# Kernel optimization log

Hardware: AMD Instinct MI355X
Metric: run time of the kernel (lower is better)

## Reference

```python
import jax, jax.numpy as jnp
import numpy as np

N, M, K, C, FF, H, OUT = 20000, 80000, 48, 64, 256, 4, 64


def _lin(x, w, b):
    return x @ w.T + b


def _bn(x, g, b, eps=1e-5):
    mu = x.mean(0)
    var = x.var(0)
    return (x - mu) * jax.lax.rsqrt(var + eps) * g + b


def setup_inputs() -> dict:
    key = jax.random.key(0)
    ks = jax.random.split(key, 24)
    voxel_features = jax.random.normal(ks[0], (M, C), jnp.float32)
    voxel_coords = jax.random.normal(ks[1], (M, 3), jnp.float32)
    query_coords = jax.random.normal(ks[2], (N, 3), jnp.float32)
    idx = jax.random.randint(ks[3], (N, K), 0, M)
    drop = jax.random.uniform(ks[4], (N, K)) < 0.1
    drop = drop.at[:, 0].set(False)  # keep >=1 valid key per query
    key_indices = jnp.where(drop, -1, idx)
    s = 0.05
    p = lambda i, shp: jax.random.normal(ks[i], shp, jnp.float32) * s
    return {
        "voxel_features": voxel_features,
        "voxel_coords": voxel_coords,
        "query_coords": query_coords,
        "key_indices": key_indices,
        "q_w": p(5, (C, 3)), "q_b": p(6, (C,)),
        "kpos_w": p(7, (C, 3)), "kpos_b": p(8, (C,)),
        "in_w": p(9, (3 * C, C)), "in_b": p(10, (3 * C,)),
        "out_w": p(11, (C, C)), "out_b": p(12, (C,)),
        "lin1_w": p(13, (FF, C)), "lin1_b": p(14, (FF,)),
        "lin2_w": p(15, (C, FF)), "lin2_b": p(16, (C,)),
        "norm_g": jnp.ones((C,), jnp.float32), "norm_b": jnp.zeros((C,), jnp.float32),
        "outl_w": p(17, (OUT, C)), "outl_b": p(18, (OUT,)),
        "obn_g": jnp.ones((OUT,), jnp.float32), "obn_b": jnp.zeros((OUT,), jnp.float32),
    }


def reference(voxel_features, voxel_coords, query_coords, key_indices,
              q_w, q_b, kpos_w, kpos_b, in_w, in_b, out_w, out_b,
              lin1_w, lin1_b, lin2_w, lin2_b, norm_g, norm_b,
              outl_w, outl_b, obn_g, obn_b):
    hd = C // H
    mask = key_indices < 0                      # (N,K) padded keys
    safe = jnp.where(mask, 0, key_indices)
    key_feats = voxel_features[safe]            # (N,K,C) hash-gather
    key_coords = voxel_coords[safe]             # (N,K,3)
    # query positional projection
    q_feat = jax.nn.relu(_lin(query_coords, q_w, q_b))          # (N,C)
    # relative coords + key positional conv1d(kernel=1) == linear on coord dim
    rel = key_coords - query_coords[:, None, :]                  # (N,K,3)
    key_feats = key_feats + jax.nn.relu(_lin(rel, kpos_w, kpos_b))
    # multihead attention, query length 1 per voxel
    Wq, Wk, Wv = jnp.split(in_w, 3, axis=0)
    bq, bk, bv = jnp.split(in_b, 3)
    q = (_lin(q_feat, Wq, bq) / jnp.sqrt(jnp.float32(hd))).reshape(N, H, hd)
    k = _lin(key_feats, Wk, bk).reshape(N, K, H, hd)
    v = _lin(key_feats, Wv, bv).reshape(N, K, H, hd)
    scores = jnp.einsum('nhd,nkhd->nhk', q, k)
    scores = jnp.where(mask[:, None, :], -jnp.inf, scores)
    attn = jax.nn.softmax(scores, axis=-1)
    ctx = jnp.einsum('nhk,nkhd->nhd', attn, v).reshape(N, C)
    att = _lin(ctx, out_w, out_b)                                # (N,C)
    # FFN + residual
    x = att + _lin(jax.nn.relu(_lin(att, lin1_w, lin1_b)), lin2_w, lin2_b)
    x = _bn(x, norm_g, norm_b)
    # output layer: Linear -> BN -> ReLU
    x = jax.nn.relu(_bn(_lin(x, outl_w, outl_b), obn_g, obn_b))
    return x
```

## Files before the change

kernel.cpp:

```cpp
#include <hip/hip_runtime.h>
#include <math.h>

#define N_Q 20000
#define KK 48
#define CC 64
#define FFD 256

#define TW_WOB   0
#define TW_WVT   4096
#define TW_L1B   8192
#define TW_L2B   16384
#define TW_OLB   24576
#define TW_QB    26624
#define TW_KB    28672
#define ST_OFF   32768
#define M_OFF    33024
#define VF_OFF   2593024

typedef short bf16x8 __attribute__((ext_vector_type(8)));
typedef float f32x4  __attribute__((ext_vector_type(4)));

__device__ __forceinline__ unsigned pk2(float a, float b) {
    unsigned r;
    asm("v_cvt_pk_bf16_f32 %0, %1, %2" : "=v"(r) : "v"(a), "v"(b));
    return r;
}
__device__ __forceinline__ unsigned f2bf(float a) {
    unsigned r;
    asm("v_cvt_pk_bf16_f32 %0, %1, 0" : "=v"(r) : "v"(a));
    return r & 0xffffu;
}
__device__ __forceinline__ float bflo(unsigned u) { return __uint_as_float(u << 16); }
__device__ __forceinline__ float bfhi(unsigned u) { return __uint_as_float(u & 0xffff0000u); }
__device__ __forceinline__ bf16x8 ldfrag(const unsigned short* p) {
    return *(const bf16x8*)p;
}

__global__ void prep_all(const float* __restrict__ in_w,
                         const float* __restrict__ out_w,
                         const float* __restrict__ lin1_w,
                         const float* __restrict__ lin2_w,
                         const float* __restrict__ outl_w,
                         const float* __restrict__ vfeat,
                         float* __restrict__ tw,
                         unsigned short* __restrict__ vfeat_bf,
                         float* __restrict__ stats)
{
    int t = blockIdx.x * 256 + threadIdx.x;
    unsigned* twu = (unsigned*)tw;
    if (t < 1280000) {
        float4 v = ((const float4*)vfeat)[t];
        uint2 p; p.x = pk2(v.x, v.y); p.y = pk2(v.z, v.w);
        ((uint2*)vfeat_bf)[t] = p;
    }
    if (t < 256) stats[t] = 0.0f;
    if (t < 4096) {
        if (t < 2048) {
            int p = t;
            int j2 = p & 3, lane = (p >> 2) & 63, nb = (p >> 8) & 3, ks = p >> 10;
            int nn = nb*16 + (lane & 15), k = ks*32 + (lane >> 4)*8 + 2*j2;
            twu[TW_WOB + p] = pk2(out_w[nn*64 + k], out_w[nn*64 + k + 1]);
        }
    } else if (t < 8192) {
        if (t < 6144) {
            int p = t - 4096;
            int j2 = p & 3, lane = (p >> 2) & 63, nb = (p >> 8) & 3, ks = p >> 10;
            int nn = nb*16 + (lane & 15), k = ks*32 + (lane >> 4)*8 + 2*j2;
            twu[TW_WVT + p] = pk2(in_w[(128 + nn)*64 + k], in_w[(128 + nn)*64 + k + 1]);
        }
    } else if (t < 16384) {
        int p = t - 8192;
        int j2 = p & 3, lane = (p >> 2) & 63, nb = (p >> 8) & 15, ks = p >> 12;
        int n = nb*16 + (lane & 15), k = ks*32 + (lane >> 4)*8 + 2*j2;
        twu[TW_L1B + p] = pk2(lin1_w[n*64 + k], lin1_w[n*64 + k + 1]);
    } else if (t < 24576) {
        int p = t - 16384;
        int j2 = p & 3, lane = (p >> 2) & 63, nb = (p >> 8) & 3, ks = p >> 10;
        int n = nb*16 + (lane & 15), k = ks*32 + (lane >> 4)*8 + 2*j2;
        twu[TW_L2B + p] = pk2(lin2_w[n*256 + k], lin2_w[n*256 + k + 1]);
    } else if (t < 26624) {
        int p = t - 24576;
        int j2 = p & 3, lane = (p >> 2) & 63, nb = (p >> 8) & 3, ks = p >> 10;
        int n = nb*16 + (lane & 15), k = ks*32 + (lane >> 4)*8 + 2*j2;
        twu[TW_OLB + p] = pk2(outl_w[n*64 + k], outl_w[n*64 + k + 1]);
    } else if (t < 28672) {
        int p = t - 26624;
        int j2 = p & 3, lane = (p >> 2) & 63, nb = (p >> 8) & 3, ks = p >> 10;
        int n = nb*16 + (lane & 15), k = ks*32 + (lane >> 4)*8 + 2*j2;
        twu[TW_QB + p] = pk2(in_w[n*64 + k], in_w[n*64 + k + 1]);
    } else if (t < 32768) {
        int p = t - 28672;
        int j2 = p & 3, lane = (p >> 2) & 63, nb = (p >> 8) & 3, h = p >> 10;
        int j = nb*16 + (lane & 15), k = (lane >> 4)*8 + 2*j2;
        unsigned u = 0;
        if (k < 16)
            u = pk2(in_w[(64 + h*16 + k)*64 + j], in_w[(64 + h*16 + k + 1)*64 + j]);
        twu[TW_KB + p] = u;
    }
}

__global__ __launch_bounds__(256) void m_kernel(
    const float* __restrict__ qcoord, const float* __restrict__ q_w,
    const float* __restrict__ q_b, const float* __restrict__ in_b,
    const float* __restrict__ tw, unsigned short* __restrict__ M_all)
{
    __shared__ __align__(16) unsigned short sQF[80*72];
    __shared__ __align__(16) unsigned short sQ[80*72];
    int t = threadIdx.x, base = blockIdx.x * 80;
    int colq = (t*4) & 63;
    float qwv[12];
    #pragma unroll
    for (int j = 0; j < 12; ++j) qwv[j] = q_w[colq*3 + j];
    float4 qb4 = *(const float4*)&q_b[colq];
    #pragma unroll
    for (int i = 0; i < 5; ++i) {
        int e = i*1024 + t*4, r = e >> 6, n = base + r;
        float c0 = qcoord[n*3], c1 = qcoord[n*3+1], c2 = qcoord[n*3+2];
        float f0 = fmaxf(fmaf(qwv[2],  c2, fmaf(qwv[1],  c1, fmaf(qwv[0], c0, qb4.x))), 0.f);
        float f1 = fmaxf(fmaf(qwv[5],  c2, fmaf(qwv[4],  c1, fmaf(qwv[3], c0, qb4.y))), 0.f);
        float f2 = fmaxf(fmaf(qwv[8],  c2, fmaf(qwv[7],  c1, fmaf(qwv[6], c0, qb4.z))), 0.f);
        float f3 = fmaxf(fmaf(qwv[11], c2, fmaf(qwv[10], c1, fmaf(qwv[9], c0, qb4.w))), 0.f);
        uint2 p; p.x = pk2(f0, f1); p.y = pk2(f2, f3);
        *(uint2*)&sQF[r*72 + colq] = p;
    }
    int w = t >> 6, lane = t & 63, l16 = lane & 15, quad = lane >> 4;
    const unsigned* QB = (const unsigned*)(tw + TW_QB);
    const unsigned* KB = (const unsigned*)(tw + TW_KB);
    bf16x8 qbf[2], kbf[4];
    #pragma unroll
    for (int ks = 0; ks < 2; ++ks)
        qbf[ks] = ldfrag((const unsigned short*)&QB[((ks*4 + w)*64 + lane)*4]);
    #pragma unroll
    for (int nb = 0; nb < 4; ++nb)
        kbf[nb] = ldfrag((const unsigned short*)&KB[((w*4 + nb)*64 + lane)*4]);
    __syncthreads();

    int cq = w*16 + l16;
    float bq = in_b[cq];
    #pragma unroll
    for (int mb = 0; mb < 5; ++mb) {
        bf16x8 a0 = ldfrag(&sQF[(mb*16 + l16)*72 + quad*8]);
        bf16x8 a1 = ldfrag(&sQF[(mb*16 + l16)*72 + 32 + quad*8]);
        f32x4 acc = {0.f, 0.f, 0.f, 0.f};
        acc = __builtin_amdgcn_mfma_f32_16x16x32_bf16(a0, qbf[0], acc, 0, 0, 0);
        acc = __builtin_amdgcn_mfma_f32_16x16x32_bf16(a1, qbf[1], acc, 0, 0, 0);
        #pragma unroll
        for (int reg = 0; reg < 4; ++reg) {
            int row = mb*16 + quad*4 + reg;
            sQ[row*72 + cq] = (unsigned short)f2bf((acc[reg] + bq) * 0.25f);
        }
    }
    #pragma unroll
    for (int mb = 0; mb < 5; ++mb) {
        bf16x8 a = {0,0,0,0,0,0,0,0};
        if (quad < 2) a = ldfrag(&sQ[(mb*16 + l16)*72 + w*16 + quad*8]);
        f32x4 acc[4];
        #pragma unroll
        for (int nb = 0; nb < 4; ++nb) {
            f32x4 z = {0.f, 0.f, 0.f, 0.f};
            acc[nb] = __builtin_amdgcn_mfma_f32_16x16x32_bf16(a, kbf[nb], z, 0, 0, 0);
        }
        #pragma unroll
        for (int nb = 0; nb < 4; ++nb)
            #pragma unroll
            for (int reg = 0; reg < 4; ++reg) {
                int r = base + mb*16 + quad*4 + reg, j = nb*16 + l16;
                M_all[(size_t)r*256 + w*64 + j] = (unsigned short)f2bf(acc[nb][reg]);
            }
    }
}

__global__ __launch_bounds__(128, 4) void attn_kernel(
    const unsigned short* __restrict__ vfeat_bf, const float* __restrict__ vcoord,
    const float* __restrict__ qcoord, const int* __restrict__ kidx,
    const float* __restrict__ kpos_w, const float* __restrict__ kpos_b,
    const float* __restrict__ in_b,
    const float* __restrict__ tw, const unsigned short* __restrict__ M_all,
    float* __restrict__ ctx_out)
{
    __shared__ __align__(16) unsigned short skf2[2][KK*72];
    int wv = threadIdx.x >> 6, c = threadIdx.x & 63;
    int n = blockIdx.x * 2 + wv;
    unsigned short* skf = skf2[wv];
    int l16 = c & 15, quad = c >> 4;

    const unsigned short* Mrow = M_all + (size_t)n*256 + (l16 & 3)*64 + quad*8;
    bf16x8 mf0 = ldfrag(Mrow);
    bf16x8 mf1 = ldfrag(Mrow + 32);
    const unsigned* VBu = (const unsigned*)(tw + TW_WVT);
    bf16x8 wvf[2][4];
    #pragma unroll
    for (int ks = 0; ks < 2; ++ks)
        #pragma unroll
        for (int nb = 0; nb < 4; ++nb)
            wvf[ks][nb] = ldfrag((const unsigned short*)&VBu[((ks*4 + nb)*64 + c)*4]);

    float qc0 = qcoord[n*3+0], qc1 = qcoord[n*3+1], qc2 = qcoord[n*3+2];

    int kread = c < 48 ? c : 47;
    int idxv = kidx[(size_t)n*KK + kread];
    int sfe = idxv < 0 ? 0 : idxv;
    float rl0 = vcoord[sfe*3+0] - qc0;
    float rl1 = vcoord[sfe*3+1] - qc1;
    float rl2 = vcoord[sfe*3+2] - qc2;

    float4 wA  = *(const float4*)(kpos_w + 12*l16 + 0);
    float4 wB  = *(const float4*)(kpos_w + 12*l16 + 4);
    float4 wC  = *(const float4*)(kpos_w + 12*l16 + 8);
    float4 kb4 = *(const float4*)(kpos_b + 4*l16);

    uint2 fv[12];
    #pragma unroll
    for (int i = 0; i < 12; ++i) {
        int row = 4*i + quad;
        int si = __shfl(idxv, row);
        si = si < 0 ? 0 : si;
        fv[i] = *(const uint2*)(vfeat_bf + (size_t)si*64 + 4*l16);
    }
    #pragma unroll
    for (int i = 0; i < 12; ++i) {
        int row = 4*i + quad;
        float rr0 = __shfl(rl0, row), rr1 = __shfl(rl1, row), rr2 = __shfl(rl2, row);
        float g0 = bflo(fv[i].x), g1 = bfhi(fv[i].x);
        float g2 = bflo(fv[i].y), g3 = bfhi(fv[i].y);
        g0 += fmaxf(fmaf(wA.x, rr0, fmaf(wA.y, rr1, fmaf(wA.z, rr2, kb4.x))), 0.0f);
        g1 += fmaxf(fmaf(wA.w, rr0, fmaf(wB.x, rr1, fmaf(wB.y, rr2, kb4.y))), 0.0f);
        g2 += fmaxf(fmaf(wB.z, rr0, fmaf(wB.w, rr1, fmaf(wC.x, rr2, kb4.z))), 0.0f);
        g3 += fmaxf(fmaf(wC.y, rr0, fmaf(wC.z, rr1, fmaf(wC.w, rr2, kb4.w))), 0.0f);
        uint2 p; p.x = pk2(g0, g1); p.y = pk2(g2, g3);
        *(uint2*)&skf[row*72 + 4*l16] = p;
    }

    unsigned long long vm = __ballot(c < 48 && idxv >= 0);
    bf16x8 a0s[3], a1s[3];
    float S[3][4];
    #pragma unroll
    for (int mb = 0; mb < 3; ++mb) {
        a0s[mb] = ldfrag(&skf[(mb*16 + l16)*72 + quad*8]);
        a1s[mb] = ldfrag(&skf[(mb*16 + l16)*72 + 32 + quad*8]);
        f32x4 acc = {0.f, 0.f, 0.f, 0.f};
        acc = __builtin_amdgcn_mfma_f32_16x16x32_bf16(a0s[mb], mf0, acc, 0, 0, 0);
        acc = __builtin_amdgcn_mfma_f32_16x16x32_bf16(a1s[mb], mf1, acc, 0, 0, 0);
        #pragma unroll
        for (int r = 0; r < 4; ++r) {
            int kk = mb*16 + quad*4 + r;
            S[mb][r] = ((vm >> kk) & 1ull) ? acc[r] : -1e30f;
        }
    }

    float mx = S[0][0];
    #pragma unroll
    for (int mb = 0; mb < 3; ++mb)
        #pragma unroll
        for (int r = 0; r < 4; ++r) mx = fmaxf(mx, S[mb][r]);
    mx = fmaxf(mx, __shfl_xor(mx, 16));
    mx = fmaxf(mx, __shfl_xor(mx, 32));
    float p[3][4], es = 0.f;
    #pragma unroll
    for (int mb = 0; mb < 3; ++mb)
        #pragma unroll
        for (int r = 0; r < 4; ++r) { p[mb][r] = __expf(S[mb][r] - mx); es += p[mb][r]; }
    es += __shfl_xor(es, 16);
    es += __shfl_xor(es, 32);
    float rinv = 1.0f / es;
    #pragma unroll
    for (int mb = 0; mb < 3; ++mb)
        #pragma unroll
        for (int r = 0; r < 4; ++r) p[mb][r] *= rinv;

    float cacc0 = 0.f, cacc1 = 0.f, cacc2 = 0.f, cacc3 = 0.f;
    #pragma unroll
    for (int mb = 0; mb < 3; ++mb) {
        f32x4 av[4];
        #pragma unroll
        for (int nb = 0; nb < 4; ++nb) {
            f32x4 z = {0.f, 0.f, 0.f, 0.f};
            z = __builtin_amdgcn_mfma_f32_16x16x32_bf16(a0s[mb], wvf[0][nb], z, 0, 0, 0);
            av[nb] = __builtin_amdgcn_mfma_f32_16x16x32_bf16(a1s[mb], wvf[1][nb], z, 0, 0, 0);
        }
        #pragma unroll
        for (int r = 0; r < 4; ++r) {
            float pv = p[mb][r];
            float p0 = __shfl(pv, quad*16 + 0);
            float p1 = __shfl(pv, quad*16 + 1);
            float p2 = __shfl(pv, quad*16 + 2);
            float p3 = __shfl(pv, quad*16 + 3);
            cacc0 = fmaf(p0, av[0][r], cacc0);
            cacc1 = fmaf(p1, av[1][r], cacc1);
            cacc2 = fmaf(p2, av[2][r], cacc2);
            cacc3 = fmaf(p3, av[3][r], cacc3);
        }
    }
    cacc0 += __shfl_xor(cacc0, 16); cacc0 += __shfl_xor(cacc0, 32);
    cacc1 += __shfl_xor(cacc1, 16); cacc1 += __shfl_xor(cacc1, 32);
    cacc2 += __shfl_xor(cacc2, 16); cacc2 += __shfl_xor(cacc2, 32);
    cacc3 += __shfl_xor(cacc3, 16); cacc3 += __shfl_xor(cacc3, 32);
    float cv = quad == 0 ? cacc0 : quad == 1 ? cacc1 : quad == 2 ? cacc2 : cacc3;
    cv += in_b[128 + c];
    ctx_out[(size_t)n*64 + c] = cv;
}

__global__ __launch_bounds__(256) void ffn_kernel(
    const float* __restrict__ tw, const float* __restrict__ out_b,
    const float* __restrict__ lin1_b, const float* __restrict__ lin2_b,
    float* __restrict__ ctx_y,
    float* __restrict__ sum1, float* __restrict__ sumsq1)
{
    __shared__ __align__(16) unsigned short sA[80*72];
    __shared__ __align__(16) unsigned short sH[80*264];
    unsigned short* sC = sH;
    int t = threadIdx.x, base = blockIdx.x * 80;
    #pragma unroll
    for (int i = 0; i < 5; ++i) {
        int e = i*1024 + t*4, r = e >> 6, col = e & 63;
        float4 v = *(const float4*)&ctx_y[(size_t)(base + r)*64 + col];
        uint2 p; p.x = pk2(v.x, v.y); p.y = pk2(v.z, v.w);
        *(uint2*)&sC[r*72 + col] = p;
    }
    int w = t >> 6, lane = t & 63, l16 = lane & 15, quad = lane >> 4;
    const unsigned* WOB = (const unsigned*)(tw + TW_WOB);
    const unsigned* L1B = (const unsigned*)(tw + TW_L1B);
    const unsigned* L2B = (const unsigned*)(tw + TW_L2B);
    bf16x8 wob[2], b1f[2][4], b2f[8];
    #pragma unroll
    for (int ks = 0; ks < 2; ++ks)
        wob[ks] = ldfrag((const unsigned short*)&WOB[((ks*4 + w)*64 + lane)*4]);
    #pragma unroll
    for (int ks = 0; ks < 2; ++ks)
        #pragma unroll
        for (int nb = 0; nb < 4; ++nb)
            b1f[ks][nb] = ldfrag((const unsigned short*)&L1B[((ks*16 + w*4 + nb)*64 + lane)*4]);
    #pragma unroll
    for (int ks = 0; ks < 8; ++ks)
        b2f[ks] = ldfrag((const unsigned short*)&L2B[((ks*4 + w)*64 + lane)*4]);
    __syncthreads();

    int c = w*16 + l16;
    float ob = out_b[c];
    f32x4 attacc[5];
    #pragma unroll
    for (int mb = 0; mb < 5; ++mb) {
        bf16x8 a0 = ldfrag(&sC[(mb*16 + l16)*72 + quad*8]);
        bf16x8 a1 = ldfrag(&sC[(mb*16 + l16)*72 + 32 + quad*8]);
        f32x4 acc = {0.f, 0.f, 0.f, 0.f};
        acc = __builtin_amdgcn_mfma_f32_16x16x32_bf16(a0, wob[0], acc, 0, 0, 0);
        acc = __builtin_amdgcn_mfma_f32_16x16x32_bf16(a1, wob[1], acc, 0, 0, 0);
        #pragma unroll
        for (int reg = 0; reg < 4; ++reg) {
            float av = acc[reg] + ob;
            attacc[mb][reg] = av;
            int row = mb*16 + quad*4 + reg;
            sA[row*72 + c] = (unsigned short)f2bf(av);
        }
    }
    __syncthreads();

    #pragma unroll
    for (int mb = 0; mb < 5; ++mb) {
        bf16x8 a0 = ldfrag(&sA[(mb*16 + l16)*72 + quad*8]);
        bf16x8 a1 = ldfrag(&sA[(mb*16 + l16)*72 + 32 + quad*8]);
        #pragma unroll
        for (int nb = 0; nb < 4; ++nb) {
            f32x4 acc = {0.f, 0.f, 0.f, 0.f};
            acc = __builtin_amdgcn_mfma_f32_16x16x32_bf16(a0, b1f[0][nb], acc, 0, 0, 0);
            acc = __builtin_amdgcn_mfma_f32_16x16x32_bf16(a1, b1f[1][nb], acc, 0, 0, 0);
            int f = w*64 + nb*16 + l16;
            float bias = lin1_b[f];
            #pragma unroll
            for (int reg = 0; reg < 4; ++reg) {
                int row = mb*16 + quad*4 + reg;
                sH[row*264 + f] = (unsigned short)f2bf(fmaxf(acc[reg] + bias, 0.0f));
            }
        }
    }
    __syncthreads();

    float lb2 = lin2_b[c];
    float s = 0.f, ss = 0.f;
    #pragma unroll
    for (int mb = 0; mb < 5; ++mb) {
        f32x4 acc = {0.f, 0.f, 0.f, 0.f};
        #pragma unroll
        for (int ks = 0; ks < 8; ++ks) {
            bf16x8 a = ldfrag(&sH[(mb*16 + l16)*264 + ks*32 + quad*8]);
            acc = __builtin_amdgcn_mfma_f32_16x16x32_bf16(a, b2f[ks], acc, 0, 0, 0);
        }
        #pragma unroll
        for (int reg = 0; reg < 4; ++reg) {
            int r = base + mb*16 + quad*4 + reg;
            float y = attacc[mb][reg] + lb2 + acc[reg];
            ctx_y[(size_t)r*64 + c] = y;
            s += y; ss = fmaf(y, y, ss);
        }
    }
    s  += __shfl_xor(s, 16);  s  += __shfl_xor(s, 32);
    ss += __shfl_xor(ss, 16); ss += __shfl_xor(ss, 32);
    if (lane < 16) {
        atomicAdd(&sum1[c], s);
        atomicAdd(&sumsq1[c], ss);
    }
}

__global__ __launch_bounds__(256) void linout_kernel(
    const float* __restrict__ tw, const float* __restrict__ outl_b,
    const float* __restrict__ norm_g, const float* __restrict__ norm_b,
    const float* __restrict__ sum1, const float* __restrict__ sumsq1,
    const float* __restrict__ y, float* __restrict__ z_out,
    float* __restrict__ sum2, float* __restrict__ sumsq2)
{
    __shared__ __align__(16) unsigned short sX[80*72];
    int t = threadIdx.x, base = blockIdx.x * 80;
    int colq = (t*4) & 63;
    const float invN = 1.0f / 20000.0f;
    float4 sm = *(const float4*)&sum1[colq];
    float4 sq = *(const float4*)&sumsq1[colq];
    float4 g  = *(const float4*)&norm_g[colq];
    float4 bb = *(const float4*)&norm_b[colq];
    float mu0 = sm.x*invN, mu1 = sm.y*invN, mu2 = sm.z*invN, mu3 = sm.w*invN;
    float a0 = g.x / sqrtf(fmaf(-mu0, mu0, sq.x*invN) + 1e-5f);
    float a1 = g.y / sqrtf(fmaf(-mu1, mu1, sq.y*invN) + 1e-5f);
    float a2 = g.z / sqrtf(fmaf(-mu2, mu2, sq.z*invN) + 1e-5f);
    float a3 = g.w / sqrtf(fmaf(-mu3, mu3, sq.w*invN) + 1e-5f);
    float b0 = fmaf(-mu0, a0, bb.x), b1 = fmaf(-mu1, a1, bb.y);
    float b2 = fmaf(-mu2, a2, bb.z), b3 = fmaf(-mu3, a3, bb.w);
    #pragma unroll
    for (int i = 0; i < 5; ++i) {
        int e = i*1024 + t*4, r = e >> 6;
        float4 v = *(const float4*)&y[(size_t)(base + r)*64 + colq];
        uint2 p;
        p.x = pk2(fmaf(v.x, a0, b0), fmaf(v.y, a1, b1));
        p.y = pk2(fmaf(v.z, a2, b2), fmaf(v.w, a3, b3));
        *(uint2*)&sX[r*72 + colq] = p;
    }
    int w = t >> 6, lane = t & 63, l16 = lane & 15, quad = lane >> 4;
    const unsigned* OLB = (const unsigned*)(tw + TW_OLB);
    bf16x8 obf[2];
    #pragma unroll
    for (int ks = 0; ks < 2; ++ks)
        obf[ks] = ldfrag((const unsigned short*)&OLB[((ks*4 + w)*64 + lane)*4]);
    __syncthreads();

    int co = w*16 + l16;
    float ob = outl_b[co];
    float s = 0.f, ss = 0.f;
    #pragma unroll
    for (int mb = 0; mb < 5; ++mb) {
        bf16x8 x0 = ldfrag(&sX[(mb*16 + l16)*72 + quad*8]);
        bf16x8 x1 = ldfrag(&sX[(mb*16 + l16)*72 + 32 + quad*8]);
        f32x4 acc = {0.f, 0.f, 0.f, 0.f};
        acc = __builtin_amdgcn_mfma_f32_16x16x32_bf16(x0, obf[0], acc, 0, 0, 0);
        acc = __builtin_amdgcn_mfma_f32_16x16x32_bf16(x1, obf[1], acc, 0, 0, 0);
        #pragma unroll
        for (int reg = 0; reg < 4; ++reg) {
            int r = base + mb*16 + quad*4 + reg;
            float zv = acc[reg] + ob;
            z_out[(size_t)r*64 + co] = zv;
            s += zv; ss = fmaf(zv, zv, ss);
        }
    }
    s  += __shfl_xor(s, 16);  s  += __shfl_xor(s, 32);
    ss += __shfl_xor(ss, 16); ss += __shfl_xor(ss, 32);
    if (lane < 16) {
        atomicAdd(&sum2[co], s);
        atomicAdd(&sumsq2[co], ss);
    }
}

__global__ void final_kernel(float* __restrict__ z,
    const float* __restrict__ sum2, const float* __restrict__ sumsq2,
    const float* __restrict__ obn_g, const float* __restrict__ obn_b)
{
    int i = blockIdx.x*blockDim.x + threadIdx.x;
    if (i >= N_Q*64/4) return;
    int o4 = (i*4) & 63;
    float4 sm = *(const float4*)&sum2[o4];
    float4 sq = *(const float4*)&sumsq2[o4];
    float4 g  = *(const float4*)&obn_g[o4];
    float4 b  = *(const float4*)&obn_b[o4];
    const float invN = 1.0f / 20000.0f;
    float mux = sm.x*invN, muy = sm.y*invN, muz = sm.z*invN, muw = sm.w*invN;
    float ax = g.x / sqrtf(fmaf(-mux, mux, sq.x*invN) + 1e-5f);
    float ay = g.y / sqrtf(fmaf(-muy, muy, sq.y*invN) + 1e-5f);
    float az = g.z / sqrtf(fmaf(-muz, muz, sq.z*invN) + 1e-5f);
    float aw = g.w / sqrtf(fmaf(-muw, muw, sq.w*invN) + 1e-5f);
    float4 v = ((float4*)z)[i];
    v.x = fmaxf(fmaf(v.x - mux, ax, b.x), 0.0f);
    v.y = fmaxf(fmaf(v.y - muy, ay, b.y), 0.0f);
    v.z = fmaxf(fmaf(v.z - muz, az, b.z), 0.0f);
    v.w = fmaxf(fmaf(v.w - muw, aw, b.w), 0.0f);
    ((float4*)z)[i] = v;
}

extern "C" void kernel_launch(void* const* d_in, const int* in_sizes, int n_in,
                              void* d_out, int out_size, void* d_ws, size_t ws_size,
                              hipStream_t stream)
{
    const float* vfeat  = (const float*)d_in[0];
    const float* vcoord = (const float*)d_in[1];
    const float* qcoord = (const float*)d_in[2];
    const int*   kidx   = (const int*)d_in[3];
    const float* q_w    = (const float*)d_in[4];
    const float* q_b    = (const float*)d_in[5];
    const float* kpos_w = (const float*)d_in[6];
    const float* kpos_b = (const float*)d_in[7];
    const float* in_w   = (const float*)d_in[8];
    const float* in_b   = (const float*)d_in[9];
    const float* out_w  = (const float*)d_in[10];
    const float* out_b  = (const float*)d_in[11];
    const float* lin1_w = (const float*)d_in[12];
    const float* lin1_b = (const float*)d_in[13];
    const float* lin2_w = (const float*)d_in[14];
    const float* lin2_b = (const float*)d_in[15];
    const float* norm_g = (const float*)d_in[16];
    const float* norm_b = (const float*)d_in[17];
    const float* outl_w = (const float*)d_in[18];
    const float* outl_b = (const float*)d_in[19];
    const float* obn_g  = (const float*)d_in[20];
    const float* obn_b  = (const float*)d_in[21];

    float* ws = (float*)d_ws;
    float* tw = ws;
    float* stats = ws + ST_OFF;
    float* sum1 = stats, *sumsq1 = stats + 64, *sum2 = stats + 128, *sumsq2 = stats + 192;
    unsigned short* M_all = (unsigned short*)(ws + M_OFF);
    unsigned short* vfeat_bf = (unsigned short*)(ws + VF_OFF);
    float* xd = (float*)d_out;

    prep_all<<<5120, 256, 0, stream>>>(in_w, out_w, lin1_w, lin2_w, outl_w,
                                       vfeat, tw, vfeat_bf, stats);
    m_kernel<<<250, 256, 0, stream>>>(qcoord, q_w, q_b, in_b, tw, M_all);
    attn_kernel<<<N_Q/2, 128, 0, stream>>>(vfeat_bf, vcoord, qcoord, kidx, kpos_w,
                                           kpos_b, in_b, tw, M_all, xd);
    ffn_kernel<<<250, 256, 0, stream>>>(tw, out_b, lin1_b, lin2_b, xd, sum1, sumsq1);
    linout_kernel<<<250, 256, 0, stream>>>(tw, outl_b, norm_g, norm_b, sum1, sumsq1,
                                           xd, xd, sum2, sumsq2);
    final_kernel<<<1250, 256, 0, stream>>>(xd, sum2, sumsq2, obn_g, obn_b);
}
```

Before: 174.9 us.

## Fuse FFN, output linear and BatchNorms into one cooperative grid-synced kernel

Merges the FFN, output-linear and final BN/ReLU kernels into a single cooperative kernel. It keeps per-block activations in registers and LDS across two grid-wide syncs, which serve as barriers for the batch-norm statistics. This removes two kernel launches and two full round trips of the intermediate activations through global memory. The attention kernel's key-feature gather also changes, from 8-byte to 16-byte loads per lane with 8 channels each. The cost is that all 250 blocks must be co-resident, and the grid syncs add barrier latency.

```diff
diff --git a/kernel.cpp b/kernel.cpp
--- a/kernel.cpp
+++ b/kernel.cpp
@@ -1,5 +1,8 @@
 #include <hip/hip_runtime.h>
+#include <hip/hip_cooperative_groups.h>
 #include <math.h>
+
+namespace cg = cooperative_groups;
 
 #define N_Q 20000
 #define KK 48
@@ -34,6 +37,9 @@
 __device__ __forceinline__ float bfhi(unsigned u) { return __uint_as_float(u & 0xffff0000u); }
 __device__ __forceinline__ bf16x8 ldfrag(const unsigned short* p) {
     return *(const bf16x8*)p;
+}
+__device__ __forceinline__ float atomld(const float* p) {
+    return __hip_atomic_load((float*)p, __ATOMIC_RELAXED, __HIP_MEMORY_SCOPE_AGENT);
 }
 
 __global__ void prep_all(const float* __restrict__ in_w,
@@ -204,31 +210,38 @@
     float rl1 = vcoord[sfe*3+1] - qc1;
     float rl2 = vcoord[sfe*3+2] - qc2;
 
-    float4 wA  = *(const float4*)(kpos_w + 12*l16 + 0);
-    float4 wB  = *(const float4*)(kpos_w + 12*l16 + 4);
-    float4 wC  = *(const float4*)(kpos_w + 12*l16 + 8);
-    float4 kb4 = *(const float4*)(kpos_b + 4*l16);
-
-    uint2 fv[12];
-    #pragma unroll
-    for (int i = 0; i < 12; ++i) {
-        int row = 4*i + quad;
+    int o8 = c >> 3, jb8 = (c & 7) * 8;
+    float w8[24], b8[8];
+    #pragma unroll
+    for (int q = 0; q < 6; ++q)
+        *(float4*)&w8[q*4] = *(const float4*)(kpos_w + jb8*3 + q*4);
+    *(float4*)&b8[0] = *(const float4*)(kpos_b + jb8);
+    *(float4*)&b8[4] = *(const float4*)(kpos_b + jb8 + 4);
+
+    uint4 fv[6];
+    #pragma unroll
+    for (int i = 0; i < 6; ++i) {
+        int row = 8*i + o8;
         int si = __shfl(idxv, row);
         si = si < 0 ? 0 : si;
-        fv[i] = *(const uint2*)(vfeat_bf + (size_t)si*64 + 4*l16);
-    }
-    #pragma unroll
-    for (int i = 0; i < 12; ++i) {
-        int row = 4*i + quad;
+        fv[i] = *(const uint4*)(vfeat_bf + (size_t)si*64 + jb8);
+    }
+    #pragma unroll
+    for (int i = 0; i < 6; ++i) {
+        int row = 8*i + o8;
         float rr0 = __shfl(rl0, row), rr1 = __shfl(rl1, row), rr2 = __shfl(rl2, row);
-        float g0 = bflo(fv[i].x), g1 = bfhi(fv[i].x);
-        float g2 = bflo(fv[i].y), g3 = bfhi(fv[i].y);
-        g0 += fmaxf(fmaf(wA.x, rr0, fmaf(wA.y, rr1, fmaf(wA.z, rr2, kb4.x))), 0.0f);
-        g1 += fmaxf(fmaf(wA.w, rr0, fmaf(wB.x, rr1, fmaf(wB.y, rr2, kb4.y))), 0.0f);
-        g2 += fmaxf(fmaf(wB.z, rr0, fmaf(wB.w, rr1, fmaf(wC.x, rr2, kb4.z))), 0.0f);
-        g3 += fmaxf(fmaf(wC.y, rr0, fmaf(wC.z, rr1, fmaf(wC.w, rr2, kb4.w))), 0.0f);
-        uint2 p; p.x = pk2(g0, g1); p.y = pk2(g2, g3);
-        *(uint2*)&skf[row*72 + 4*l16] = p;
+        unsigned uu[4] = {fv[i].x, fv[i].y, fv[i].z, fv[i].w};
+        unsigned pp[4];
+        #pragma unroll
+        for (int q2 = 0; q2 < 4; ++q2) {
+            int k0 = 2*q2, k1 = 2*q2 + 1;
+            float gl = bflo(uu[q2]), gh = bfhi(uu[q2]);
+            gl += fmaxf(fmaf(w8[3*k0+2], rr2, fmaf(w8[3*k0+1], rr1, fmaf(w8[3*k0], rr0, b8[k0]))), 0.f);
+            gh += fmaxf(fmaf(w8[3*k1+2], rr2, fmaf(w8[3*k1+1], rr1, fmaf(w8[3*k1], rr0, b8[k1]))), 0.f);
+            pp[q2] = pk2(gl, gh);
+        }
+        uint4 st; st.x = pp[0]; st.y = pp[1]; st.z = pp[2]; st.w = pp[3];
+        *(uint4*)&skf[row*72 + jb8] = st;
     }
 
     unsigned long long vm = __ballot(c < 48 && idxv >= 0);
@@ -300,20 +313,28 @@
     ctx_out[(size_t)n*64 + c] = cv;
 }
 
-__global__ __launch_bounds__(256) void ffn_kernel(
+__global__ __launch_bounds__(256) void fused_tail(
     const float* __restrict__ tw, const float* __restrict__ out_b,
     const float* __restrict__ lin1_b, const float* __restrict__ lin2_b,
-    float* __restrict__ ctx_y,
-    float* __restrict__ sum1, float* __restrict__ sumsq1)
+    const float* __restrict__ norm_g, const float* __restrict__ norm_b,
+    const float* __restrict__ outl_b, const float* __restrict__ obn_g,
+    const float* __restrict__ obn_b, float* __restrict__ xd,
+    float* __restrict__ sum1, float* __restrict__ sumsq1,
+    float* __restrict__ sum2, float* __restrict__ sumsq2)
 {
+    cg::grid_group grid = cg::this_grid();
     __shared__ __align__(16) unsigned short sA[80*72];
     __shared__ __align__(16) unsigned short sH[80*264];
     unsigned short* sC = sH;
+    float*          sY = (float*)sH;
+    unsigned short* sX = sA;
     int t = threadIdx.x, base = blockIdx.x * 80;
+    const float invN = 1.0f / 20000.0f;
+
     #pragma unroll
     for (int i = 0; i < 5; ++i) {
         int e = i*1024 + t*4, r = e >> 6, col = e & 63;
-        float4 v = *(const float4*)&ctx_y[(size_t)(base + r)*64 + col];
+        float4 v = *(const float4*)&xd[(size_t)(base + r)*64 + col];
         uint2 p; p.x = pk2(v.x, v.y); p.y = pk2(v.z, v.w);
         *(uint2*)&sC[r*72 + col] = p;
     }
@@ -321,6 +342,7 @@
     const unsigned* WOB = (const unsigned*)(tw + TW_WOB);
     const unsigned* L1B = (const unsigned*)(tw + TW_L1B);
     const unsigned* L2B = (const unsigned*)(tw + TW_L2B);
+    const unsigned* OLB = (const unsigned*)(tw + TW_OLB);
     bf16x8 wob[2], b1f[2][4], b2f[8];
     #pragma unroll
     for (int ks = 0; ks < 2; ++ks)
@@ -387,9 +409,8 @@
         }
         #pragma unroll
         for (int reg = 0; reg < 4; ++reg) {
-            int r = base + mb*16 + quad*4 + reg;
             float y = attacc[mb][reg] + lb2 + acc[reg];
-            ctx_y[(size_t)r*64 + c] = y;
+            attacc[mb][reg] = y;
             s += y; ss = fmaf(y, y, ss);
         }
     }
@@ -399,50 +420,47 @@
         atomicAdd(&sum1[c], s);
         atomicAdd(&sumsq1[c], ss);
     }
-}
-
-__global__ __launch_bounds__(256) void linout_kernel(
-    const float* __restrict__ tw, const float* __restrict__ outl_b,
-    const float* __restrict__ norm_g, const float* __restrict__ norm_b,
-    const float* __restrict__ sum1, const float* __restrict__ sumsq1,
-    const float* __restrict__ y, float* __restrict__ z_out,
-    float* __restrict__ sum2, float* __restrict__ sumsq2)
-{
-    __shared__ __align__(16) unsigned short sX[80*72];
-    int t = threadIdx.x, base = blockIdx.x * 80;
+    __syncthreads();
+    #pragma unroll
+    for (int mb = 0; mb < 5; ++mb)
+        #pragma unroll
+        for (int reg = 0; reg < 4; ++reg)
+            sY[(mb*16 + quad*4 + reg)*64 + c] = attacc[mb][reg];
+    __threadfence();
+    grid.sync();
+
     int colq = (t*4) & 63;
-    const float invN = 1.0f / 20000.0f;
-    float4 sm = *(const float4*)&sum1[colq];
-    float4 sq = *(const float4*)&sumsq1[colq];
+    float sm0 = atomld(&sum1[colq]),   sm1 = atomld(&sum1[colq+1]);
+    float sm2 = atomld(&sum1[colq+2]), sm3 = atomld(&sum1[colq+3]);
+    float sq0 = atomld(&sumsq1[colq]),   sq1 = atomld(&sumsq1[colq+1]);
+    float sq2 = atomld(&sumsq1[colq+2]), sq3 = atomld(&sumsq1[colq+3]);
     float4 g  = *(const float4*)&norm_g[colq];
     float4 bb = *(const float4*)&norm_b[colq];
-    float mu0 = sm.x*invN, mu1 = sm.y*invN, mu2 = sm.z*invN, mu3 = sm.w*invN;
-    float a0 = g.x / sqrtf(fmaf(-mu0, mu0, sq.x*invN) + 1e-5f);
-    float a1 = g.y / sqrtf(fmaf(-mu1, mu1, sq.y*invN) + 1e-5f);
-    float a2 = g.z / sqrtf(fmaf(-mu2, mu2, sq.z*invN) + 1e-5f);
-    float a3 = g.w / sqrtf(fmaf(-mu3, mu3, sq.w*invN) + 1e-5f);
+    float mu0 = sm0*invN, mu1 = sm1*invN, mu2 = sm2*invN, mu3 = sm3*invN;
+    float a0 = g.x / sqrtf(fmaf(-mu0, mu0, sq0*invN) + 1e-5f);
+    float a1 = g.y / sqrtf(fmaf(-mu1, mu1, sq1*invN) + 1e-5f);
+    float a2 = g.z / sqrtf(fmaf(-mu2, mu2, sq2*invN) + 1e-5f);
+    float a3 = g.w / sqrtf(fmaf(-mu3, mu3, sq3*invN) + 1e-5f);
     float b0 = fmaf(-mu0, a0, bb.x), b1 = fmaf(-mu1, a1, bb.y);
     float b2 = fmaf(-mu2, a2, bb.z), b3 = fmaf(-mu3, a3, bb.w);
     #pragma unroll
     for (int i = 0; i < 5; ++i) {
         int e = i*1024 + t*4, r = e >> 6;
-        float4 v = *(const float4*)&y[(size_t)(base + r)*64 + colq];
+        float4 v = *(const float4*)&sY[r*64 + colq];
         uint2 p;
         p.x = pk2(fmaf(v.x, a0, b0), fmaf(v.y, a1, b1));
         p.y = pk2(fmaf(v.z, a2, b2), fmaf(v.w, a3, b3));
         *(uint2*)&sX[r*72 + colq] = p;
     }
-    int w = t >> 6, lane = t & 63, l16 = lane & 15, quad = lane >> 4;
-    const unsigned* OLB = (const unsigned*)(tw + TW_OLB);
     bf16x8 obf[2];
     #pragma unroll
     for (int ks = 0; ks < 2; ++ks)
         obf[ks] = ldfrag((const unsigned short*)&OLB[((ks*4 + w)*64 + lane)*4]);
     __syncthreads();
 
-    int co = w*16 + l16;
-    float ob = outl_b[co];
-    float s = 0.f, ss = 0.f;
+    float obv = outl_b[c];
+    f32x4 zacc[5];
+    float s2 = 0.f, ss2 = 0.f;
     #pragma unroll
     for (int mb = 0; mb < 5; ++mb) {
         bf16x8 x0 = ldfrag(&sX[(mb*16 + l16)*72 + quad*8]);
@@ -452,43 +470,31 @@
         acc = __builtin_amdgcn_mfma_f32_16x16x32_bf16(x1, obf[1], acc, 0, 0, 0);
         #pragma unroll
         for (int reg = 0; reg < 4; ++reg) {
+            float zv = acc[reg] + obv;
+            zacc[mb][reg] = zv;
+            s2 += zv; ss2 = fmaf(zv, zv, ss2);
+        }
+    }
+    s2  += __shfl_xor(s2, 16);  s2  += __shfl_xor(s2, 32);
+    ss2 += __shfl_xor(ss2, 16); ss2 += __shfl_xor(ss2, 32);
+    if (lane < 16) {
+        atomicAdd(&sum2[c], s2);
+        atomicAdd(&sumsq2[c], ss2);
+    }
+    __threadfence();
+    grid.sync();
+
+    float smz = atomld(&sum2[c]), sqz = atomld(&sumsq2[c]);
+    float muz = smz*invN;
+    float az = obn_g[c] / sqrtf(fmaf(-muz, muz, sqz*invN) + 1e-5f);
+    float bz = fmaf(-muz, az, obn_b[c]);
+    #pragma unroll
+    for (int mb = 0; mb < 5; ++mb)
+        #pragma unroll
+        for (int reg = 0; reg < 4; ++reg) {
             int r = base + mb*16 + quad*4 + reg;
-            float zv = acc[reg] + ob;
-            z_out[(size_t)r*64 + co] = zv;
-            s += zv; ss = fmaf(zv, zv, ss);
-        }
-    }
-    s  += __shfl_xor(s, 16);  s  += __shfl_xor(s, 32);
-    ss += __shfl_xor(ss, 16); ss += __shfl_xor(ss, 32);
-    if (lane < 16) {
-        atomicAdd(&sum2[co], s);
-        atomicAdd(&sumsq2[co], ss);
-    }
-}
-
-__global__ void final_kernel(float* __restrict__ z,
-    const float* __restrict__ sum2, const float* __restrict__ sumsq2,
-    const float* __restrict__ obn_g, const float* __restrict__ obn_b)
-{
-    int i = blockIdx.x*blockDim.x + threadIdx.x;
-    if (i >= N_Q*64/4) return;
-    int o4 = (i*4) & 63;
-    float4 sm = *(const float4*)&sum2[o4];
-    float4 sq = *(const float4*)&sumsq2[o4];
-    float4 g  = *(const float4*)&obn_g[o4];
-    float4 b  = *(const float4*)&obn_b[o4];
-    const float invN = 1.0f / 20000.0f;
-    float mux = sm.x*invN, muy = sm.y*invN, muz = sm.z*invN, muw = sm.w*invN;
-    float ax = g.x / sqrtf(fmaf(-mux, mux, sq.x*invN) + 1e-5f);
-    float ay = g.y / sqrtf(fmaf(-muy, muy, sq.y*invN) + 1e-5f);
-    float az = g.z / sqrtf(fmaf(-muz, muz, sq.z*invN) + 1e-5f);
-    float aw = g.w / sqrtf(fmaf(-muw, muw, sq.w*invN) + 1e-5f);
-    float4 v = ((float4*)z)[i];
-    v.x = fmaxf(fmaf(v.x - mux, ax, b.x), 0.0f);
-    v.y = fmaxf(fmaf(v.y - muy, ay, b.y), 0.0f);
-    v.z = fmaxf(fmaf(v.z - muz, az, b.z), 0.0f);
-    v.w = fmaxf(fmaf(v.w - muw, aw, b.w), 0.0f);
-    ((float4*)z)[i] = v;
+            xd[(size_t)r*64 + c] = fmaxf(fmaf(zacc[mb][reg], az, bz), 0.0f);
+        }
 }
 
 extern "C" void kernel_launch(void* const* d_in, const int* in_sizes, int n_in,
@@ -531,8 +537,12 @@
     m_kernel<<<250, 256, 0, stream>>>(qcoord, q_w, q_b, in_b, tw, M_all);
     attn_kernel<<<N_Q/2, 128, 0, stream>>>(vfeat_bf, vcoord, qcoord, kidx, kpos_w,
                                            kpos_b, in_b, tw, M_all, xd);
-    ffn_kernel<<<250, 256, 0, stream>>>(tw, out_b, lin1_b, lin2_b, xd, sum1, sumsq1);
-    linout_kernel<<<250, 256, 0, stream>>>(tw, outl_b, norm_g, norm_b, sum1, sumsq1,
-                                           xd, xd, sum2, sumsq2);
-    final_kernel<<<1250, 256, 0, stream>>>(xd, sum2, sumsq2, obn_g, obn_b);
-}
+    {
+        void* args[] = { (void*)&tw, (void*)&out_b, (void*)&lin1_b, (void*)&lin2_b,
+                         (void*)&norm_g, (void*)&norm_b, (void*)&outl_b,
+                         (void*)&obn_g, (void*)&obn_b, (void*)&xd,
+                         (void*)&sum1, (void*)&sumsq1, (void*)&sum2, (void*)&sumsq2 };
+        hipLaunchCooperativeKernel((const void*)fused_tail, dim3(250), dim3(256),
+                                   args, 0, stream);
+    }
+}
```

New measurement: 269.0 us. +53.8%, slower.
